# Performance work log

Hardware: AMD Instinct MI355X
Metric: run time of the kernel (lower is better)

The kernel has to match this reference:

```python
import jax, jax.numpy as jnp
import numpy as np

def setup_inputs() -> dict:
    key = jax.random.key(0)
    k1, k2 = jax.random.split(key)
    B, T, J, d = 128, 2048, 128, 512
    U = jax.random.normal(k1, (B, J, d), dtype=jnp.float32)  # query encoding
    S = jax.random.normal(k2, (B, T, J), dtype=jnp.float32)  # similarity matrix
    return {"U": U, "S": S}

def reference(U, S):
    # a = softmax(S) over last (query) axis; out[b,t,:] = sum_j a[b,t,j] * U[b,j,:]
    # The original expand_dims/multiply/sum is algebraically a batched matmul.
    a = jax.nn.softmax(S, axis=-1)          # [B, T, J]
    return jnp.einsum('btj,bjd->btd', a, U)  # [B, T, d]
```

## Files before the change

### kernel.cpp

```cpp
#include <hip/hip_runtime.h>
#include <stdint.h>

typedef uint16_t u16;
typedef uint32_t u32;
typedef __attribute__((ext_vector_type(4))) int   int4v;
typedef __attribute__((ext_vector_type(4))) short short4v;
typedef __attribute__((ext_vector_type(8))) short short8;
typedef __attribute__((ext_vector_type(4))) float float4v;

__device__ __forceinline__ u16 f2bf(float f) {
  u32 x = __float_as_uint(f);
  x += 0x7fffu + ((x >> 16) & 1u);
  return (u16)(x >> 16);
}
__device__ __forceinline__ void llds16(const u16* g, u16* l) {
  __builtin_amdgcn_global_load_lds(
      (const __attribute__((address_space(1))) void*)g,
      (__attribute__((address_space(3))) void*)l, 16, 0, 0);
}

#define BB 128
#define TT 2048
#define JJ 128
#define DD 512

__global__ __launch_bounds__(256) void u_transpose(const float* __restrict__ U,
                                                   u16* __restrict__ Ut) {
  __shared__ u16 tile[128 * 72];
  const int t  = threadIdx.x;
  const int b  = blockIdx.x >> 3;
  const int d0 = (blockIdx.x & 7) << 6;
  const float* src = U + (size_t)b * (JJ * DD);
  u16* dst         = Ut + (size_t)b * (DD * JJ);
#pragma unroll
  for (int i = 0; i < 8; ++i) {
    int idx = i * 256 + t;
    int j = idx >> 4, c = idx & 15;
    float4v v = *(const float4v*)(src + (size_t)j * DD + d0 + c * 4);
    short4v p;
#pragma unroll
    for (int e = 0; e < 4; ++e) p[e] = (short)f2bf(v[e]);
    *(short4v*)(tile + j * 72 + c * 4) = p;
  }
  __syncthreads();
#pragma unroll
  for (int i = 0; i < 4; ++i) {
    int idx = i * 256 + t;
    int n = idx >> 4, cj = idx & 15;
    short8 vv;
#pragma unroll
    for (int k = 0; k < 8; ++k) vv[k] = (short)tile[(cj * 8 + k) * 72 + n];
    *(short8*)(dst + (size_t)(d0 + n) * JJ + cj * 8) = vv;
  }
}

__global__ __launch_bounds__(256, 2) void softmax_gemm(const float* __restrict__ S,
                                                       const u16* __restrict__ Ut,
                                                       float* __restrict__ O) {
  __shared__ __align__(16) char smem[128 * 132 * 4];
  u16* a_lds   = (u16*)smem;
  u16* b_lds   = (u16*)(smem + 32768);
  float* o_lds = (float*)smem;

  const int tid = threadIdx.x;
  const int bi  = blockIdx.x;
  const int tn  = bi & 3;
  const int tm  = (bi >> 2) & 15;
  const int b   = bi >> 6;
  const int wave = tid >> 6;
  const int lane = tid & 63;

  {
    const u16* utb = Ut + ((size_t)b * DD + tn * 128) * JJ;
#pragma unroll
    for (int i = 0; i < 8; ++i) {
      int ch = i * 256 + tid;
      int s = ch >> 9, n = (ch >> 2) & 127, c4 = ch & 3;
      const u16* g = utb + n * JJ + s * 32 + c4 * 8;
      u16* l = b_lds + (size_t)(i * 256 + wave * 64) * 8;
      llds16(g, l);
    }
  }

  const int m = tid >> 1, h = tid & 1;
  const float* srow = S + ((size_t)b * TT + tm * 128 + m) * JJ + h * 64;
  float x[64];
#pragma unroll
  for (int c = 0; c < 16; ++c) {
    float4v v = ((const float4v*)srow)[c];
#pragma unroll
    for (int e = 0; e < 4; ++e) x[c * 4 + e] = v[e];
  }
  float mx = -1e30f;
#pragma unroll
  for (int e = 0; e < 64; ++e) mx = fmaxf(mx, x[e]);
  mx = fmaxf(mx, __shfl_xor(mx, 1, 64));
  float sum = 0.f;
#pragma unroll
  for (int e = 0; e < 64; ++e) { x[e] = __expf(x[e] - mx); sum += x[e]; }
  sum += __shfl_xor(sum, 1, 64);
  const float rs = 1.0f / sum;
#pragma unroll
  for (int c = 0; c < 8; ++c) {
    short8 us;
#pragma unroll
    for (int e = 0; e < 8; ++e) us[e] = (short)f2bf(x[c * 8 + e] * rs);
    int s  = h * 2 + (c >> 2);
    int qp = (c & 3) ^ ((m >> 1) & 3);
    *(short8*)(a_lds + s * 4096 + m * 32 + qp * 8) = us;
  }

  __syncthreads();

  const int wm = wave & 1, wn = wave >> 1;
  const int ml = lane & 15, quad = lane >> 4;

  float4v acc[4][4];
#pragma unroll
  for (int mi = 0; mi < 4; ++mi)
#pragma unroll
    for (int ni = 0; ni < 4; ++ni) {
      float4v z = {0.f, 0.f, 0.f, 0.f};
      acc[mi][ni] = z;
    }

#pragma unroll
  for (int s = 0; s < 4; ++s) {
    short8 av[4], bv[4];
#pragma unroll
    for (int mi = 0; mi < 4; ++mi) {
      int mm = wm * 64 + mi * 16 + ml;
      int qp = quad ^ ((mm >> 1) & 3);
      av[mi] = *(const short8*)(a_lds + s * 4096 + mm * 32 + qp * 8);
    }
#pragma unroll
    for (int ni = 0; ni < 4; ++ni) {
      int nn = wn * 64 + ni * 16 + ml;
      bv[ni] = *(const short8*)(b_lds + s * 4096 + nn * 32 + quad * 8);
    }
#pragma unroll
    for (int mi = 0; mi < 4; ++mi)
#pragma unroll
      for (int ni = 0; ni < 4; ++ni)
        acc[mi][ni] = __builtin_amdgcn_mfma_f32_16x16x32_bf16(av[mi], bv[ni],
                                                              acc[mi][ni], 0, 0, 0);
  }

  __syncthreads();

#pragma unroll
  for (int mi = 0; mi < 4; ++mi) {
    int row0 = wm * 64 + mi * 16 + quad * 4;
#pragma unroll
    for (int ni = 0; ni < 4; ++ni) {
      int col = wn * 64 + ni * 16 + ml;
#pragma unroll
      for (int rr = 0; rr < 4; ++rr)
        o_lds[(row0 + rr) * 132 + col] = acc[mi][ni][rr];
    }
  }
  __syncthreads();

  float* ob = O + ((size_t)b * TT + tm * 128) * DD + tn * 128;
#pragma unroll
  for (int i = 0; i < 16; ++i) {
    int ch = i * 256 + tid;
    int row = ch >> 5, c = ch & 31;
    *(float4v*)(ob + (size_t)row * DD + c * 4) =
        *(const float4v*)(o_lds + row * 132 + c * 4);
  }
}

extern "C" void kernel_launch(void* const* d_in, const int* in_sizes, int n_in,
                              void* d_out, int out_size, void* d_ws, size_t ws_size,
                              hipStream_t stream) {
  (void)in_sizes; (void)n_in; (void)out_size; (void)ws_size;
  const float* U = (const float*)d_in[0];
  const float* S = (const float*)d_in[1];
  float* out = (float*)d_out;
  u16* Ut    = (u16*)d_ws;

  u_transpose<<<BB * 8, 256, 0, stream>>>(U, Ut);
  softmax_gemm<<<BB * 16 * 4, 256, 0, stream>>>(S, Ut, out);
}
```

Measured before the change: 684.1 us.

## Compute softmax once per row tile and loop over all output column tiles

Each block now owns a full 128-row tile of T and loops over all four 128-wide d tiles. This removes the fourfold redundant reading and softmax of S that the old grid did. The next Ut tile is prefetched into registers while the current one is computed, and the B tile in LDS is XOR-swizzled. The MFMA operands are swapped so results are stored straight to global as float4 without the LDS staging pass. Block indices are also swizzled for locality. In exchange there are fewer blocks (2048), extra registers for the prefetch and A fragments, and more barriers per block.

```diff
diff --git a/kernel.cpp b/kernel.cpp
--- a/kernel.cpp
+++ b/kernel.cpp
@@ -57,29 +57,37 @@
 __global__ __launch_bounds__(256, 2) void softmax_gemm(const float* __restrict__ S,
                                                        const u16* __restrict__ Ut,
                                                        float* __restrict__ O) {
-  __shared__ __align__(16) char smem[128 * 132 * 4];
-  u16* a_lds   = (u16*)smem;
-  u16* b_lds   = (u16*)(smem + 32768);
-  float* o_lds = (float*)smem;
+  __shared__ __align__(16) u16 a_lds[128 * 128];
+  __shared__ __align__(16) u16 b_lds[128 * 128];
 
   const int tid = threadIdx.x;
-  const int bi  = blockIdx.x;
-  const int tn  = bi & 3;
-  const int tm  = (bi >> 2) & 15;
-  const int b   = bi >> 6;
-  const int wave = tid >> 6;
-  const int lane = tid & 63;
-
-  {
-    const u16* utb = Ut + ((size_t)b * DD + tn * 128) * JJ;
-#pragma unroll
-    for (int i = 0; i < 8; ++i) {
-      int ch = i * 256 + tid;
-      int s = ch >> 9, n = (ch >> 2) & 127, c4 = ch & 3;
-      const u16* g = utb + n * JJ + s * 32 + c4 * 8;
-      u16* l = b_lds + (size_t)(i * 256 + wave * 64) * 8;
-      llds16(g, l);
-    }
+  const int bid = blockIdx.x;
+  const int swz = (bid & 7) * 256 + (bid >> 3);
+  const int b   = swz >> 4;
+  const int tm  = swz & 15;
+  const int wave = tid >> 6, lane = tid & 63;
+  const int ml = lane & 15, quad = lane >> 4;
+  const int wm = wave & 1, wn = wave >> 1;
+
+  const u16* utb = Ut + (size_t)b * (DD * JJ);
+
+#pragma unroll
+  for (int i = 0; i < 8; ++i) {
+    int ch = i * 256 + tid;
+    int s = ch >> 9, n = (ch >> 2) & 127, qp = ch & 3;
+    int c4 = qp ^ ((n >> 1) & 3);
+    const u16* g = utb + n * JJ + s * 32 + c4 * 8;
+    u16* l = b_lds + (size_t)(i * 256 + wave * 64) * 8;
+    llds16(g, l);
+  }
+
+  int4v pf[8];
+#pragma unroll
+  for (int i = 0; i < 8; ++i) {
+    int ch = i * 256 + tid;
+    int s = ch >> 9, n = (ch >> 2) & 127, qp = ch & 3;
+    int c4 = qp ^ ((n >> 1) & 3);
+    pf[i] = *(const int4v*)(utb + (size_t)128 * JJ + n * JJ + s * 32 + c4 * 8);
   }
 
   const int m = tid >> 1, h = tid & 1;
@@ -112,62 +120,75 @@
 
   __syncthreads();
 
-  const int wm = wave & 1, wn = wave >> 1;
-  const int ml = lane & 15, quad = lane >> 4;
-
-  float4v acc[4][4];
-#pragma unroll
-  for (int mi = 0; mi < 4; ++mi)
-#pragma unroll
-    for (int ni = 0; ni < 4; ++ni) {
-      float4v z = {0.f, 0.f, 0.f, 0.f};
-      acc[mi][ni] = z;
+  short8 av[4][4];
+#pragma unroll
+  for (int mi = 0; mi < 4; ++mi) {
+    int mm = wm * 64 + mi * 16 + ml;
+    int qp = quad ^ ((mm >> 1) & 3);
+#pragma unroll
+    for (int s = 0; s < 4; ++s)
+      av[mi][s] = *(const short8*)(a_lds + s * 4096 + mm * 32 + qp * 8);
+  }
+
+  float* ob = O + ((size_t)b * TT + tm * 128) * DD;
+
+#pragma unroll
+  for (int tn = 0; tn < 4; ++tn) {
+    float4v acc[4][4];
+#pragma unroll
+    for (int mi = 0; mi < 4; ++mi)
+#pragma unroll
+      for (int ni = 0; ni < 4; ++ni) {
+        float4v z = {0.f, 0.f, 0.f, 0.f};
+        acc[mi][ni] = z;
+      }
+
+#pragma unroll
+    for (int s = 0; s < 4; ++s) {
+      short8 bv[4];
+#pragma unroll
+      for (int ni = 0; ni < 4; ++ni) {
+        int nn = wn * 64 + ni * 16 + ml;
+        int qp = quad ^ ((nn >> 1) & 3);
+        bv[ni] = *(const short8*)(b_lds + s * 4096 + nn * 32 + qp * 8);
+      }
+#pragma unroll
+      for (int mi = 0; mi < 4; ++mi)
+#pragma unroll
+        for (int ni = 0; ni < 4; ++ni)
+          acc[mi][ni] = __builtin_amdgcn_mfma_f32_16x16x32_bf16(
+              bv[ni], av[mi][s], acc[mi][ni], 0, 0, 0);
     }
 
-#pragma unroll
-  for (int s = 0; s < 4; ++s) {
-    short8 av[4], bv[4];
+    if (tn < 3) {
+      __syncthreads();
+#pragma unroll
+      for (int i = 0; i < 8; ++i) {
+        int ch = i * 256 + tid;
+        *(int4v*)(b_lds + (size_t)ch * 8) = pf[i];
+      }
+      __syncthreads();
+      if (tn < 2) {
+        const u16* utn = utb + (size_t)(tn + 2) * 128 * JJ;
+#pragma unroll
+        for (int i = 0; i < 8; ++i) {
+          int ch = i * 256 + tid;
+          int s = ch >> 9, n = (ch >> 2) & 127, qp = ch & 3;
+          int c4 = qp ^ ((n >> 1) & 3);
+          pf[i] = *(const int4v*)(utn + n * JJ + s * 32 + c4 * 8);
+        }
+      }
+    }
+
 #pragma unroll
     for (int mi = 0; mi < 4; ++mi) {
-      int mm = wm * 64 + mi * 16 + ml;
-      int qp = quad ^ ((mm >> 1) & 3);
-      av[mi] = *(const short8*)(a_lds + s * 4096 + mm * 32 + qp * 8);
+      const int t = wm * 64 + mi * 16 + ml;
+#pragma unroll
+      for (int ni = 0; ni < 4; ++ni) {
+        const int d = tn * 128 + wn * 64 + ni * 16 + quad * 4;
+        *(float4v*)(ob + (size_t)t * DD + d) = acc[mi][ni];
+      }
     }
-#pragma unroll
-    for (int ni = 0; ni < 4; ++ni) {
-      int nn = wn * 64 + ni * 16 + ml;
-      bv[ni] = *(const short8*)(b_lds + s * 4096 + nn * 32 + quad * 8);
-    }
-#pragma unroll
-    for (int mi = 0; mi < 4; ++mi)
-#pragma unroll
-      for (int ni = 0; ni < 4; ++ni)
-        acc[mi][ni] = __builtin_amdgcn_mfma_f32_16x16x32_bf16(av[mi], bv[ni],
-                                                              acc[mi][ni], 0, 0, 0);
-  }
-
-  __syncthreads();
-
-#pragma unroll
-  for (int mi = 0; mi < 4; ++mi) {
-    int row0 = wm * 64 + mi * 16 + quad * 4;
-#pragma unroll
-    for (int ni = 0; ni < 4; ++ni) {
-      int col = wn * 64 + ni * 16 + ml;
-#pragma unroll
-      for (int rr = 0; rr < 4; ++rr)
-        o_lds[(row0 + rr) * 132 + col] = acc[mi][ni][rr];
-    }
-  }
-  __syncthreads();
-
-  float* ob = O + ((size_t)b * TT + tm * 128) * DD + tn * 128;
-#pragma unroll
-  for (int i = 0; i < 16; ++i) {
-    int ch = i * 256 + tid;
-    int row = ch >> 5, c = ch & 31;
-    *(float4v*)(ob + (size_t)row * DD + c * 4) =
-        *(const float4v*)(o_lds + row * 132 + c * 4);
   }
 }
 
@@ -181,5 +202,5 @@
   u16* Ut    = (u16*)d_ws;
 
   u_transpose<<<BB * 8, 256, 0, stream>>>(U, Ut);
-  softmax_gemm<<<BB * 16 * 4, 256, 0, stream>>>(S, Ut, out);
-}
+  softmax_gemm<<<BB * 16, 256, 0, stream>>>(S, Ut, out);
+}
```

Measured after the change: 663.0 us. 1.03x faster.
